# Optimization experiments

Measured on AMD Instinct MI355X. Metric: run time of the kernel, lower is better.

The kernel has to match this reference:

```python
import jax, jax.numpy as jnp
import numpy as np

N = 50000      # nodes
E = 600000     # edges
DIN = 128      # input_dim
H = 128        # hidden_dim
NH = 8         # heads
HD = H // NH   # head_dim = 16
OUT = 128      # output_dim
P = 20000      # pos/neg pair count
EPS = 1e-5


def setup_inputs() -> dict:
    key = jax.random.key(0)
    ks = jax.random.split(key, 20)
    s = 0.05
    inp = {
        "x": jax.random.normal(ks[0], (N, DIN), jnp.float32),
        "edge_index": jax.random.randint(ks[1], (2, E), 0, N),
        "drug_pos_ids": jax.random.randint(ks[2], (P,), 0, N),
        "target_pos_ids": jax.random.randint(ks[3], (P,), 0, N),
        "drug_neg_ids": jax.random.randint(ks[4], (P,), 0, N),
        "target_neg_ids": jax.random.randint(ks[5], (P,), 0, N),
        "adjacency_matrix": jnp.zeros((1,), jnp.float32),  # unused by forward
        # GCN weights stored [in, out]; biases [out]
        "gcn_w0": jax.random.normal(ks[6], (DIN, H), jnp.float32) * s,
        "gcn_b0": jnp.zeros((H,), jnp.float32),
        "gcn_w1": jax.random.normal(ks[7], (H, H), jnp.float32) * s,
        "gcn_b1": jnp.zeros((H,), jnp.float32),
        "gcn_w2": jax.random.normal(ks[8], (H, H), jnp.float32) * s,
        "gcn_b2": jnp.zeros((H,), jnp.float32),
        "wq": jax.random.normal(ks[9], (H, H), jnp.float32) * s,
        "wk": jax.random.normal(ks[10], (H, H), jnp.float32) * s,
        "wv": jax.random.normal(ks[11], (H, H), jnp.float32) * s,
        "ln_g": jnp.ones((H,), jnp.float32),   # shared LayerNorm (same instance reused)
        "ln_b": jnp.zeros((H,), jnp.float32),
        "out_w": jax.random.normal(ks[12], (H, OUT), jnp.float32) * s,
        "out_b": jnp.zeros((OUT,), jnp.float32),
    }
    return inp


def _layernorm(t, g, b):
    mu = t.mean(-1, keepdims=True)
    var = ((t - mu) ** 2).mean(-1, keepdims=True)
    return (t - mu) * jax.lax.rsqrt(var + EPS) * g + b


def reference(x, edge_index, drug_pos_ids, target_pos_ids, drug_neg_ids, target_neg_ids,
              adjacency_matrix, gcn_w0, gcn_b0, gcn_w1, gcn_b1, gcn_w2, gcn_b2,
              wq, wk, wv, ln_g, ln_b, out_w, out_b):
    num_nodes = x.shape[0]
    loop = jnp.arange(num_nodes)
    src = jnp.concatenate([edge_index[0], loop])  # add self-loops (PyG GCNConv default)
    dst = jnp.concatenate([edge_index[1], loop])
    deg = jax.ops.segment_sum(jnp.ones_like(dst, dtype=x.dtype), dst, num_segments=num_nodes)
    dinv = jnp.where(deg > 0, jax.lax.rsqrt(deg), 0.0)
    norm = dinv[src] * dinv[dst]  # [E+N]

    def gcn(h, W, b):
        hw = h @ W                                    # [N,H]
        msg = hw[src] * norm[:, None]                 # gather + scale  [E+N,H]
        return jax.ops.segment_sum(msg, dst, num_segments=num_nodes) + b

    cur = x
    embs = []
    for W, b in ((gcn_w0, gcn_b0), (gcn_w1, gcn_b1), (gcn_w2, gcn_b2)):
        new = jnp.maximum(gcn(cur, W, b), 0.0)
        new = _layernorm(new, ln_g, ln_b)
        # dropout is identity in eval mode
        cur = cur + new if cur.shape == new.shape else new
        embs.append(cur)
    emb = jnp.stack(embs, axis=0)  # [L,N,H]
    L = emb.shape[0]

    def split_heads(t):  # [L,N,H] -> [NH,N,L,HD]
        return t.reshape(L, num_nodes, NH, HD).transpose(2, 1, 0, 3)

    q = split_heads(emb @ wq)
    k = split_heads(emb @ wk)
    v = split_heads(emb @ wv)
    scores = jnp.einsum('hnld,hnmd->hnlm', q, k) / jnp.sqrt(jnp.float32(HD))
    attn = jax.nn.softmax(scores, axis=-1)  # dropout = identity in eval
    ctx = jnp.einsum('hnlm,hnmd->hnld', attn, v)          # [NH,N,L,HD]
    ctx = ctx.transpose(2, 1, 0, 3).reshape(L, num_nodes, H)

    z = _layernorm(ctx, ln_g, ln_b)
    z_last = z[-1] @ out_w + out_b  # [N,OUT]; z_D == z_T in original code
    return (z_last[drug_pos_ids], z_last[target_pos_ids],
            z_last[drug_neg_ids], z_last[target_neg_ids])
```

## Files before the change

kernel.cpp:

```cpp
#include <hip/hip_runtime.h>
#include <math.h>

using bf16x8 = __attribute__((ext_vector_type(8))) short;
using f32x4  = __attribute__((ext_vector_type(4))) float;

__device__ __forceinline__ unsigned short f2b(float f) {
  unsigned u = __float_as_uint(f);
  u += 0x7FFFu + ((u >> 16) & 1u);
  return (unsigned short)(u >> 16);
}
__device__ __forceinline__ float b2f(unsigned short h) {
  return __uint_as_float((unsigned)h << 16);
}
__device__ __forceinline__ float2 upk(unsigned u) {
  return make_float2(__uint_as_float(u << 16), __uint_as_float(u & 0xFFFF0000u));
}


__global__ void k_degree(const int* __restrict__ dst, int* __restrict__ degi, int E) {
  int e = blockIdx.x * blockDim.x + threadIdx.x;
  if (e < E) atomicAdd(&degi[dst[e]], 1);
}

__global__ void k_dinv(const int* __restrict__ degi, float* __restrict__ dinv, int n) {
  int i = blockIdx.x * blockDim.x + threadIdx.x;
  if (i < n) dinv[i] = rsqrtf((float)(degi[i] + 1));
}

__global__ __launch_bounds__(256)
void k_part(const int* __restrict__ deg, int* __restrict__ part, int n) {
  __shared__ int l[256];
  int tid = threadIdx.x, i = blockIdx.x * 256 + tid;
  l[tid] = (i < n) ? deg[i] : 0;
  __syncthreads();
  for (int s = 128; s; s >>= 1) { if (tid < s) l[tid] += l[tid + s]; __syncthreads(); }
  if (!tid) part[blockIdx.x] = l[0];
}

__global__ __launch_bounds__(1024)
void k_scanpart(int* __restrict__ part, int np, int* __restrict__ off_n) {
  __shared__ int l[1024];
  int tid = threadIdx.x;
  int v = (tid < np) ? part[tid] : 0;
  l[tid] = v;
  __syncthreads();
  for (int s = 1; s < 1024; s <<= 1) {
    int t = (tid >= s) ? l[tid - s] : 0;
    __syncthreads();
    l[tid] += t;
    __syncthreads();
  }
  if (tid < np) part[tid] = l[tid] - v;
  if (tid == np - 1) *off_n = l[tid];
}

__global__ __launch_bounds__(256)
void k_off(const int* __restrict__ deg, const int* __restrict__ part,
           int* __restrict__ off, int n) {
  __shared__ int l[256];
  int tid = threadIdx.x, i = blockIdx.x * 256 + tid;
  int v = (i < n) ? deg[i] : 0;
  l[tid] = v;
  __syncthreads();
  for (int s = 1; s < 256; s <<= 1) {
    int t = (tid >= s) ? l[tid - s] : 0;
    __syncthreads();
    l[tid] += t;
    __syncthreads();
  }
  if (i < n) off[i] = part[blockIdx.x] + l[tid] - v;
}

__global__ void k_scatter(const int* __restrict__ srcv, const int* __restrict__ dstv,
                          const float* __restrict__ dinv, const int* __restrict__ off,
                          int* __restrict__ cursor, int* __restrict__ csr_src,
                          float* __restrict__ csr_norm, int E) {
  int e = blockIdx.x * blockDim.x + threadIdx.x;
  if (e >= E) return;
  int d = dstv[e];
  int p = atomicAdd(&cursor[d], 1);
  int slot = off[d] + p;
  int s = srcv[e];
  csr_src[slot] = s;
  csr_norm[slot] = dinv[s] * dinv[d];
}


__global__ void k_cvtx(const float* __restrict__ x, unsigned short* __restrict__ xb,
                       long n4) {
  long t = (long)blockIdx.x * blockDim.x + threadIdx.x;
  if (t >= n4) return;
  float4 v = ((const float4*)x)[t];
  unsigned lo = (unsigned)f2b(v.x) | ((unsigned)f2b(v.y) << 16);
  unsigned hi = (unsigned)f2b(v.z) | ((unsigned)f2b(v.w) << 16);
  ((uint2*)xb)[t] = make_uint2(lo, hi);
}


__global__ __launch_bounds__(256)
void k_cvtw(const float* gw0, const float* gw1, const float* gw2,
            const float* wk, const float* wv, const float* wq, const float* ow,
            unsigned short* gwT0, unsigned short* gwT1, unsigned short* gwT2,
            unsigned short* wkvT, unsigned short* wqT, unsigned short* owT) {
  const float* src; unsigned short* dst;
  switch (blockIdx.y) {
    case 0: src = gw0; dst = gwT0; break;
    case 1: src = gw1; dst = gwT1; break;
    case 2: src = gw2; dst = gwT2; break;
    case 3: src = wk;  dst = wkvT; break;
    case 4: src = wv;  dst = wkvT + 128 * 128; break;
    case 5: src = wq;  dst = wqT; break;
    default: src = ow; dst = owT; break;
  }
  int t = blockIdx.x * 256 + threadIdx.x;
  int r = t >> 7, c = t & 127;
  dst[(long)c * 128 + r] = f2b(src[t]);
}


__global__ __launch_bounds__(128, 6)
void k_gcn_layer(const unsigned short* __restrict__ embp,
                 const int* __restrict__ off, const int* __restrict__ csr_src,
                 const float* __restrict__ csr_norm, const float* __restrict__ dinv,
                 const unsigned short* __restrict__ wT,
                 const float* __restrict__ bias,
                 const float* __restrict__ ln_g, const float* __restrict__ ln_b,
                 unsigned short* __restrict__ embo, int N) {
  __shared__ unsigned a_sw[16 * 64];
  __shared__ float lnsum[16][2], lnsq[16][2];

  int tid = threadIdx.x, lane = tid & 63, w = tid >> 6;
  int g = lane >> 4, c16 = lane & 15;
  long n0 = (long)blockIdx.x * 16;

  for (int t = 0; t < 8; ++t) {
    int row = w * 8 + t;
    long node = n0 + row;
    long nc = node < N ? node : N - 1;
    float dn = dinv[nc];
    int s0 = off[nc], s1 = off[nc + 1];
    float acc[8];
    {
      uint4 rs_ = *(const uint4*)&embp[nc * 128 + c16 * 8];
      float wgt = (g == 0) ? dn * dn : 0.f;
      float2 f;
      f = upk(rs_.x); acc[0] = f.x * wgt; acc[1] = f.y * wgt;
      f = upk(rs_.y); acc[2] = f.x * wgt; acc[3] = f.y * wgt;
      f = upk(rs_.z); acc[4] = f.x * wgt; acc[5] = f.y * wgt;
      f = upk(rs_.w); acc[6] = f.x * wgt; acc[7] = f.y * wgt;
    }
    for (int i = s0; i < s1; i += 16) {
      int id[4]; float nm[4];
#pragma unroll
      for (int u = 0; u < 4; ++u) {
        int j = i + u * 4 + g;
        int jj = j < s1 ? j : s1 - 1;
        id[u] = csr_src[jj];
        nm[u] = j < s1 ? csr_norm[jj] : 0.f;
      }
      uint4 rv[4];
#pragma unroll
      for (int u = 0; u < 4; ++u)
        rv[u] = *(const uint4*)&embp[(long)id[u] * 128 + c16 * 8];
#pragma unroll
      for (int u = 0; u < 4; ++u) {
        float2 f0 = upk(rv[u].x), f1 = upk(rv[u].y);
        float2 f2 = upk(rv[u].z), f3 = upk(rv[u].w);
        acc[0] += f0.x * nm[u]; acc[1] += f0.y * nm[u];
        acc[2] += f1.x * nm[u]; acc[3] += f1.y * nm[u];
        acc[4] += f2.x * nm[u]; acc[5] += f2.y * nm[u];
        acc[6] += f3.x * nm[u]; acc[7] += f3.y * nm[u];
      }
    }
#pragma unroll
    for (int k = 0; k < 8; ++k) {
      acc[k] += __shfl_xor(acc[k], 16);
      acc[k] += __shfl_xor(acc[k], 32);
    }
    if (g == 0) {
      unsigned* dst = (unsigned*)((char*)a_sw +
                      (row * 256 + ((c16 * 16) ^ ((row & 7) << 4))));
      dst[0] = (unsigned)f2b(acc[0]) | ((unsigned)f2b(acc[1]) << 16);
      dst[1] = (unsigned)f2b(acc[2]) | ((unsigned)f2b(acc[3]) << 16);
      dst[2] = (unsigned)f2b(acc[4]) | ((unsigned)f2b(acc[5]) << 16);
      dst[3] = (unsigned)f2b(acc[6]) | ((unsigned)f2b(acc[7]) << 16);
    }
  }
  __syncthreads();

  int lo = lane & 15, hi = lane >> 4;
  int cb0 = w * 64;
  f32x4 acc2[4] = {};
#pragma unroll
  for (int ks = 0; ks < 4; ++ks) {
    int k0 = ks * 32 + hi * 8;
    bf16x8 a = *(const bf16x8*)((char*)a_sw + lo * 256 + ((k0 * 2) ^ ((lo & 7) << 4)));
#pragma unroll
    for (int cf = 0; cf < 4; ++cf) {
      bf16x8 b = *(const bf16x8*)&wT[(long)(cb0 + cf * 16 + lo) * 128 + k0];
      acc2[cf] = __builtin_amdgcn_mfma_f32_16x16x32_bf16(a, b, acc2[cf], 0, 0, 0);
    }
  }

  float vreg[4][4];
#pragma unroll
  for (int j = 0; j < 4; ++j) {
    float s = 0.f, q = 0.f;
#pragma unroll
    for (int cf = 0; cf < 4; ++cf) {
      int col = cb0 + cf * 16 + lo;
      float v = fmaxf(acc2[cf][j] + bias[col], 0.f);
      vreg[cf][j] = v;
      s += v; q += v * v;
    }
#pragma unroll
    for (int m = 1; m < 16; m <<= 1) { s += __shfl_xor(s, m); q += __shfl_xor(q, m); }
    if (lo == 0) { lnsum[hi * 4 + j][w] = s; lnsq[hi * 4 + j][w] = q; }
  }
  __syncthreads();
#pragma unroll
  for (int j = 0; j < 4; ++j) {
    int row = hi * 4 + j;
    float sum = lnsum[row][0] + lnsum[row][1];
    float sq  = lnsq[row][0] + lnsq[row][1];
    float mu = sum * (1.f / 128.f);
    float var = sq * (1.f / 128.f) - mu * mu;
    float rs = rsqrtf(var + 1e-5f);
    long gr = n0 + row;
    if (gr < N) {
#pragma unroll
      for (int cf = 0; cf < 4; ++cf) {
        int col = cb0 + cf * 16 + lo;
        float z = (vreg[cf][j] - mu) * rs * ln_g[col] + ln_b[col]
                  + b2f(embp[gr * 128 + col]);
        embo[gr * 128 + col] = f2b(z);
      }
    }
  }
}


__global__ __launch_bounds__(256)
void k_attn_fused(const unsigned short* __restrict__ emb,
                  const unsigned short* __restrict__ wkvT,
                  const unsigned short* __restrict__ wqT,
                  const unsigned short* __restrict__ owT,
                  const float* __restrict__ ln_g, const float* __restrict__ ln_b,
                  const float* __restrict__ out_b,
                  float* __restrict__ zout, int N) {
  __shared__ unsigned short kvl[48 * 256];
  __shared__ unsigned short ql[16 * 128];
  __shared__ unsigned short zl[16 * 128];

  int tid = threadIdx.x, lane = tid & 63, w = tid >> 6;
  int lo = lane & 15, hi = lane >> 4;
  long n0 = (long)blockIdx.x * 16;
  long nr = n0 + lo; if (nr >= N) nr = N - 1;

  {
    int cb0 = w * 64;
    f32x4 acc[3][4] = {};
#pragma unroll
    for (int ks = 0; ks < 4; ++ks) {
      int k0 = ks * 32 + hi * 8;
      bf16x8 a[3];
#pragma unroll
      for (int l = 0; l < 3; ++l)
        a[l] = *(const bf16x8*)&emb[((long)l * N + nr) * 128 + k0];
#pragma unroll
      for (int cf = 0; cf < 4; ++cf) {
        bf16x8 b = *(const bf16x8*)&wkvT[(long)(cb0 + cf * 16 + lo) * 128 + k0];
#pragma unroll
        for (int l = 0; l < 3; ++l)
          acc[l][cf] = __builtin_amdgcn_mfma_f32_16x16x32_bf16(a[l], b, acc[l][cf], 0, 0, 0);
      }
    }
#pragma unroll
    for (int l = 0; l < 3; ++l)
#pragma unroll
      for (int cf = 0; cf < 4; ++cf)
#pragma unroll
        for (int j = 0; j < 4; ++j)
          kvl[(l * 16 + hi * 4 + j) * 256 + cb0 + cf * 16 + lo] = f2b(acc[l][cf][j]);
  }

  {
    int cq0 = w * 32;
    f32x4 aq[2] = {};
#pragma unroll
    for (int ks = 0; ks < 4; ++ks) {
      int k0 = ks * 32 + hi * 8;
      bf16x8 a = *(const bf16x8*)&emb[(2L * N + nr) * 128 + k0];
#pragma unroll
      for (int cf = 0; cf < 2; ++cf) {
        bf16x8 b = *(const bf16x8*)&wqT[(long)(cq0 + cf * 16 + lo) * 128 + k0];
        aq[cf] = __builtin_amdgcn_mfma_f32_16x16x32_bf16(a, b, aq[cf], 0, 0, 0);
      }
    }
#pragma unroll
    for (int cf = 0; cf < 2; ++cf)
#pragma unroll
      for (int j = 0; j < 4; ++j)
        ql[(hi * 4 + j) * 128 + cq0 + cf * 16 + lo] = f2b(aq[cf][j]);
  }
  __syncthreads();

  {
    const unsigned* kvu = (const unsigned*)kvl;
    const unsigned* qu  = (const unsigned*)ql;
    int c = lane * 2;
    float gx = ln_g[c], gy = ln_g[c + 1], bx = ln_b[c], by = ln_b[c + 1];
#pragma unroll
    for (int it = 0; it < 4; ++it) {
      int node = w * 4 + it;
      float2 q = upk(qu[node * 64 + lane]);
      float s[3], vx[3], vy[3];
#pragma unroll
      for (int m = 0; m < 3; ++m) {
        int row = m * 16 + node;
        float2 k = upk(kvu[row * 128 + lane]);
        float2 v = upk(kvu[row * 128 + 64 + lane]);
        float p = q.x * k.x + q.y * k.y;
        p += __shfl_xor(p, 1); p += __shfl_xor(p, 2); p += __shfl_xor(p, 4);
        s[m] = p * 0.25f;
        vx[m] = v.x; vy[m] = v.y;
      }
      float mx = fmaxf(s[0], fmaxf(s[1], s[2]));
      float e0 = __expf(s[0] - mx), e1 = __expf(s[1] - mx), e2 = __expf(s[2] - mx);
      float inv = 1.f / (e0 + e1 + e2);
      float cx = (e0 * vx[0] + e1 * vx[1] + e2 * vx[2]) * inv;
      float cy = (e0 * vy[0] + e1 * vy[1] + e2 * vy[2]) * inv;
      float sum = cx + cy, sq = cx * cx + cy * cy;
#pragma unroll
      for (int m = 1; m < 64; m <<= 1) { sum += __shfl_xor(sum, m); sq += __shfl_xor(sq, m); }
      float mu = sum * (1.f / 128.f);
      float var = sq * (1.f / 128.f) - mu * mu;
      float rs = rsqrtf(var + 1e-5f);
      unsigned pk = (unsigned)f2b((cx - mu) * rs * gx + bx) |
                    ((unsigned)f2b((cy - mu) * rs * gy + by) << 16);
      *(unsigned*)((char*)zl + node * 256 + ((lane * 4) ^ ((node & 7) << 4))) = pk;
    }
  }
  __syncthreads();

  {
    int co0 = w * 32;
    f32x4 ao[2] = {};
#pragma unroll
    for (int ks = 0; ks < 4; ++ks) {
      int k0 = ks * 32 + hi * 8;
      bf16x8 a = *(const bf16x8*)((const char*)zl + lo * 256 + (((k0 * 2) ^ ((lo & 7) << 4))));
#pragma unroll
      for (int cf = 0; cf < 2; ++cf) {
        bf16x8 b = *(const bf16x8*)&owT[(long)(co0 + cf * 16 + lo) * 128 + k0];
        ao[cf] = __builtin_amdgcn_mfma_f32_16x16x32_bf16(a, b, ao[cf], 0, 0, 0);
      }
    }
#pragma unroll
    for (int cf = 0; cf < 2; ++cf)
#pragma unroll
      for (int j = 0; j < 4; ++j) {
        long gn = n0 + hi * 4 + j;
        int col = co0 + cf * 16 + lo;
        if (gn < N) zout[gn * 128 + col] = ao[cf][j] + out_b[col];
      }
  }
}


__global__ void k_gather4(const float* __restrict__ zout,
                          const int* __restrict__ ids0, const int* __restrict__ ids1,
                          const int* __restrict__ ids2, const int* __restrict__ ids3,
                          float* __restrict__ outp, int rows) {
  int t = blockIdx.x * blockDim.x + threadIdx.x;
  if (t >= rows * 32) return;
  int s = blockIdx.y;
  const int* ids = (s == 0) ? ids0 : (s == 1) ? ids1 : (s == 2) ? ids2 : ids3;
  int row = t >> 5, c4 = t & 31;
  long id = ids[row];
  ((float4*)outp)[((long)s * rows + row) * 32 + c4] = ((const float4*)zout)[id * 32 + c4];
}


extern "C" void kernel_launch(void* const* d_in, const int* in_sizes, int n_in,
                              void* d_out, int out_size, void* d_ws, size_t ws_size,
                              hipStream_t stream) {
  const float* x = (const float*)d_in[0];
  const int* ei = (const int*)d_in[1];
  const int* ids[4] = {(const int*)d_in[2], (const int*)d_in[3],
                       (const int*)d_in[4], (const int*)d_in[5]};
  const float* gw[3] = {(const float*)d_in[7], (const float*)d_in[9], (const float*)d_in[11]};
  const float* gb[3] = {(const float*)d_in[8], (const float*)d_in[10], (const float*)d_in[12]};
  const float* wq = (const float*)d_in[13];
  const float* wk = (const float*)d_in[14];
  const float* wv = (const float*)d_in[15];
  const float* ln_g = (const float*)d_in[16];
  const float* ln_b = (const float*)d_in[17];
  const float* out_w = (const float*)d_in[18];
  const float* out_b = (const float*)d_in[19];

  const int N = in_sizes[0] / 128;
  const int E = in_sizes[1] / 2;
  const int P = in_sizes[2];

  char* w = (char*)d_ws;
  size_t o = 0;
  auto take = [&](size_t bytes) -> void* {
    void* p = w + o;
    o = (o + bytes + 255) & ~(size_t)255;
    return p;
  };
  int*   degi    = (int*)take((size_t)N * 4);
  int*   off     = (int*)take((size_t)(N + 1) * 4);
  int*   cursor  = (int*)take((size_t)N * 4);
  int*   part    = (int*)take(1024 * 4);
  float* dinv    = (float*)take((size_t)N * 4);
  int*   csr_src = (int*)take((size_t)E * 4);
  float* csr_nrm = (float*)take((size_t)E * 4);
  unsigned short* gwT0 = (unsigned short*)take(128 * 128 * 2);
  unsigned short* gwT1 = (unsigned short*)take(128 * 128 * 2);
  unsigned short* gwT2 = (unsigned short*)take(128 * 128 * 2);
  unsigned short* wkvT = (unsigned short*)take(256 * 128 * 2);
  unsigned short* wqT  = (unsigned short*)take(128 * 128 * 2);
  unsigned short* owT  = (unsigned short*)take(128 * 128 * 2);
  unsigned short* xbf  = (unsigned short*)take((size_t)N * 128 * 2);
  unsigned short* emball = (unsigned short*)take((size_t)3 * N * 128 * 2);
  float* zout = (float*)take((size_t)N * 128 * 4);
  (void)ws_size; (void)n_in; (void)out_size;

  hipMemsetAsync(degi, 0, (size_t)N * 4, stream);
  hipMemsetAsync(cursor, 0, (size_t)N * 4, stream);

  int eb = (E + 255) / 256;
  int nb = (N + 255) / 256;
  k_degree<<<eb, 256, 0, stream>>>(ei + E, degi, E);
  k_dinv<<<nb, 256, 0, stream>>>(degi, dinv, N);
  k_part<<<nb, 256, 0, stream>>>(degi, part, N);
  k_scanpart<<<1, 1024, 0, stream>>>(part, nb, off + N);
  k_off<<<nb, 256, 0, stream>>>(degi, part, off, N);
  k_scatter<<<eb, 256, 0, stream>>>(ei, ei + E, dinv, off, cursor, csr_src, csr_nrm, E);
  k_cvtw<<<dim3(64, 7), 256, 0, stream>>>(gw[0], gw[1], gw[2], wk, wv, wq, out_w,
                                          gwT0, gwT1, gwT2, wkvT, wqT, owT);
  long n4 = (long)N * 32;
  k_cvtx<<<(int)((n4 + 255) / 256), 256, 0, stream>>>(x, xbf, n4);

  unsigned short* gwT[3] = {gwT0, gwT1, gwT2};
  int lgrid = (N + 15) / 16;
  const unsigned short* prev = xbf;
  for (int l = 0; l < 3; ++l) {
    unsigned short* outp = emball + (size_t)l * N * 128;
    k_gcn_layer<<<lgrid, 128, 0, stream>>>(prev, off, csr_src, csr_nrm, dinv,
                                           gwT[l], gb[l], ln_g, ln_b, outp, N);
    prev = outp;
  }

  k_attn_fused<<<(N + 15) / 16, 256, 0, stream>>>(emball, wkvT, wqT, owT,
                                                  ln_g, ln_b, out_b, zout, N);

  float* outf = (float*)d_out;
  int gb2 = (P * 32 + 255) / 256;
  k_gather4<<<dim3(gb2, 4), 256, 0, stream>>>(zout, ids[0], ids[1], ids[2], ids[3],
                                              outf, P);
}
```

Before: 308.6 us.

## Rework GCN gather to 256-thread blocks, prefetch attention loads, swizzle LDS

The GCN layer kernel moves from 128 to 256 threads per block. Each wave now processes 4 rows, with every lane gathering 2 columns over 16 neighbours at once instead of 16-byte vectors split across 4 neighbour groups, and the MFMA/LayerNorm epilogue is split across 4 waves. The attention kernel double-buffers its K/V operand loads across k-steps, reuses the layer-2 embedding fragments for the Q projection instead of reloading them, and XOR-swizzles the kv/q LDS layout to reduce bank conflicts. The gather change trades larger vector loads for more independent loads in flight, and the extra prefetch registers may reduce occupancy.

```diff
diff --git a/kernel.cpp b/kernel.cpp
--- a/kernel.cpp
+++ b/kernel.cpp
@@ -118,7 +118,7 @@
 }
 
 
-__global__ __launch_bounds__(128, 6)
+__global__ __launch_bounds__(256)
 void k_gcn_layer(const unsigned short* __restrict__ embp,
                  const int* __restrict__ off, const int* __restrict__ csr_src,
                  const float* __restrict__ csr_norm, const float* __restrict__ dinv,
@@ -127,87 +127,64 @@
                  const float* __restrict__ ln_g, const float* __restrict__ ln_b,
                  unsigned short* __restrict__ embo, int N) {
   __shared__ unsigned a_sw[16 * 64];
-  __shared__ float lnsum[16][2], lnsq[16][2];
+  __shared__ float lnsum[16][4], lnsq[16][4];
 
   int tid = threadIdx.x, lane = tid & 63, w = tid >> 6;
-  int g = lane >> 4, c16 = lane & 15;
   long n0 = (long)blockIdx.x * 16;
-
-  for (int t = 0; t < 8; ++t) {
-    int row = w * 8 + t;
+  int c = lane * 2;
+
+  for (int t = 0; t < 4; ++t) {
+    int row = w * 4 + t;
     long node = n0 + row;
-    long nc = node < N ? node : N - 1;
-    float dn = dinv[nc];
-    int s0 = off[nc], s1 = off[nc + 1];
-    float acc[8];
-    {
-      uint4 rs_ = *(const uint4*)&embp[nc * 128 + c16 * 8];
-      float wgt = (g == 0) ? dn * dn : 0.f;
-      float2 f;
-      f = upk(rs_.x); acc[0] = f.x * wgt; acc[1] = f.y * wgt;
-      f = upk(rs_.y); acc[2] = f.x * wgt; acc[3] = f.y * wgt;
-      f = upk(rs_.z); acc[4] = f.x * wgt; acc[5] = f.y * wgt;
-      f = upk(rs_.w); acc[6] = f.x * wgt; acc[7] = f.y * wgt;
-    }
+    if (node >= N) node = N - 1;
+    float dn = dinv[node];
+    float2 acc = upk(*(const unsigned*)&embp[node * 128 + c]);
+    acc.x *= dn * dn; acc.y *= dn * dn;
+    int s0 = off[node], s1 = off[node + 1];
     for (int i = s0; i < s1; i += 16) {
-      int id[4]; float nm[4];
-#pragma unroll
-      for (int u = 0; u < 4; ++u) {
-        int j = i + u * 4 + g;
-        int jj = j < s1 ? j : s1 - 1;
-        id[u] = csr_src[jj];
-        nm[u] = j < s1 ? csr_norm[jj] : 0.f;
-      }
-      uint4 rv[4];
-#pragma unroll
-      for (int u = 0; u < 4; ++u)
-        rv[u] = *(const uint4*)&embp[(long)id[u] * 128 + c16 * 8];
-#pragma unroll
-      for (int u = 0; u < 4; ++u) {
-        float2 f0 = upk(rv[u].x), f1 = upk(rv[u].y);
-        float2 f2 = upk(rv[u].z), f3 = upk(rv[u].w);
-        acc[0] += f0.x * nm[u]; acc[1] += f0.y * nm[u];
-        acc[2] += f1.x * nm[u]; acc[3] += f1.y * nm[u];
-        acc[4] += f2.x * nm[u]; acc[5] += f2.y * nm[u];
-        acc[6] += f3.x * nm[u]; acc[7] += f3.y * nm[u];
-      }
-    }
-#pragma unroll
-    for (int k = 0; k < 8; ++k) {
-      acc[k] += __shfl_xor(acc[k], 16);
-      acc[k] += __shfl_xor(acc[k], 32);
-    }
-    if (g == 0) {
-      unsigned* dst = (unsigned*)((char*)a_sw +
-                      (row * 256 + ((c16 * 16) ^ ((row & 7) << 4))));
-      dst[0] = (unsigned)f2b(acc[0]) | ((unsigned)f2b(acc[1]) << 16);
-      dst[1] = (unsigned)f2b(acc[2]) | ((unsigned)f2b(acc[3]) << 16);
-      dst[2] = (unsigned)f2b(acc[4]) | ((unsigned)f2b(acc[5]) << 16);
-      dst[3] = (unsigned)f2b(acc[6]) | ((unsigned)f2b(acc[7]) << 16);
-    }
+      int idx[16]; float nrm[16];
+#pragma unroll
+      for (int u = 0; u < 16; ++u) {
+        int j = (i + u < s1) ? i + u : s1 - 1;
+        idx[u] = csr_src[j];
+        nrm[u] = (i + u < s1) ? csr_norm[j] : 0.f;
+      }
+      unsigned rv[16];
+#pragma unroll
+      for (int u = 0; u < 16; ++u)
+        rv[u] = *(const unsigned*)&embp[(long)idx[u] * 128 + c];
+#pragma unroll
+      for (int u = 0; u < 16; ++u) {
+        float2 f = upk(rv[u]);
+        acc.x += f.x * nrm[u];
+        acc.y += f.y * nrm[u];
+      }
+    }
+    unsigned pk = (unsigned)f2b(acc.x) | ((unsigned)f2b(acc.y) << 16);
+    *(unsigned*)((char*)a_sw + row * 256 + ((lane * 4) ^ ((row & 7) << 4))) = pk;
   }
   __syncthreads();
 
   int lo = lane & 15, hi = lane >> 4;
-  int cb0 = w * 64;
-  f32x4 acc2[4] = {};
+  int cb0 = w * 32;
+  f32x4 acc2[2] = {};
 #pragma unroll
   for (int ks = 0; ks < 4; ++ks) {
     int k0 = ks * 32 + hi * 8;
     bf16x8 a = *(const bf16x8*)((char*)a_sw + lo * 256 + ((k0 * 2) ^ ((lo & 7) << 4)));
 #pragma unroll
-    for (int cf = 0; cf < 4; ++cf) {
+    for (int cf = 0; cf < 2; ++cf) {
       bf16x8 b = *(const bf16x8*)&wT[(long)(cb0 + cf * 16 + lo) * 128 + k0];
       acc2[cf] = __builtin_amdgcn_mfma_f32_16x16x32_bf16(a, b, acc2[cf], 0, 0, 0);
     }
   }
 
-  float vreg[4][4];
+  float vreg[2][4];
 #pragma unroll
   for (int j = 0; j < 4; ++j) {
     float s = 0.f, q = 0.f;
 #pragma unroll
-    for (int cf = 0; cf < 4; ++cf) {
+    for (int cf = 0; cf < 2; ++cf) {
       int col = cb0 + cf * 16 + lo;
       float v = fmaxf(acc2[cf][j] + bias[col], 0.f);
       vreg[cf][j] = v;
@@ -221,15 +198,15 @@
 #pragma unroll
   for (int j = 0; j < 4; ++j) {
     int row = hi * 4 + j;
-    float sum = lnsum[row][0] + lnsum[row][1];
-    float sq  = lnsq[row][0] + lnsq[row][1];
+    float sum = lnsum[row][0] + lnsum[row][1] + lnsum[row][2] + lnsum[row][3];
+    float sq  = lnsq[row][0] + lnsq[row][1] + lnsq[row][2] + lnsq[row][3];
     float mu = sum * (1.f / 128.f);
     float var = sq * (1.f / 128.f) - mu * mu;
     float rs = rsqrtf(var + 1e-5f);
     long gr = n0 + row;
     if (gr < N) {
 #pragma unroll
-      for (int cf = 0; cf < 4; ++cf) {
+      for (int cf = 0; cf < 2; ++cf) {
         int col = cb0 + cf * 16 + lo;
         float z = (vreg[cf][j] - mu) * rs * ln_g[col] + ln_b[col]
                   + b2f(embp[gr * 128 + col]);
@@ -257,22 +234,45 @@
   long n0 = (long)blockIdx.x * 16;
   long nr = n0 + lo; if (nr >= N) nr = N - 1;
 
+  bf16x8 a2k[4];
+
   {
     int cb0 = w * 64;
     f32x4 acc[3][4] = {};
-#pragma unroll
-    for (int ks = 0; ks < 4; ++ks) {
-      int k0 = ks * 32 + hi * 8;
-      bf16x8 a[3];
+    bf16x8 a[3], b[4];
+    {
+      int k0 = hi * 8;
 #pragma unroll
       for (int l = 0; l < 3; ++l)
         a[l] = *(const bf16x8*)&emb[((long)l * N + nr) * 128 + k0];
 #pragma unroll
-      for (int cf = 0; cf < 4; ++cf) {
-        bf16x8 b = *(const bf16x8*)&wkvT[(long)(cb0 + cf * 16 + lo) * 128 + k0];
+      for (int cf = 0; cf < 4; ++cf)
+        b[cf] = *(const bf16x8*)&wkvT[(long)(cb0 + cf * 16 + lo) * 128 + k0];
+    }
+    a2k[0] = a[2];
+#pragma unroll
+    for (int ks = 0; ks < 4; ++ks) {
+      bf16x8 an[3], bn[4];
+      if (ks < 3) {
+        int k1 = (ks + 1) * 32 + hi * 8;
 #pragma unroll
         for (int l = 0; l < 3; ++l)
-          acc[l][cf] = __builtin_amdgcn_mfma_f32_16x16x32_bf16(a[l], b, acc[l][cf], 0, 0, 0);
+          an[l] = *(const bf16x8*)&emb[((long)l * N + nr) * 128 + k1];
+#pragma unroll
+        for (int cf = 0; cf < 4; ++cf)
+          bn[cf] = *(const bf16x8*)&wkvT[(long)(cb0 + cf * 16 + lo) * 128 + k1];
+      }
+#pragma unroll
+      for (int cf = 0; cf < 4; ++cf)
+#pragma unroll
+        for (int l = 0; l < 3; ++l)
+          acc[l][cf] = __builtin_amdgcn_mfma_f32_16x16x32_bf16(a[l], b[cf], acc[l][cf], 0, 0, 0);
+      if (ks < 3) {
+#pragma unroll
+        for (int l = 0; l < 3; ++l) a[l] = an[l];
+#pragma unroll
+        for (int cf = 0; cf < 4; ++cf) b[cf] = bn[cf];
+        a2k[ks + 1] = a[2];
       }
     }
 #pragma unroll
@@ -280,8 +280,12 @@
 #pragma unroll
       for (int cf = 0; cf < 4; ++cf)
 #pragma unroll
-        for (int j = 0; j < 4; ++j)
-          kvl[(l * 16 + hi * 4 + j) * 256 + cb0 + cf * 16 + lo] = f2b(acc[l][cf][j]);
+        for (int j = 0; j < 4; ++j) {
+          int row = l * 16 + hi * 4 + j;
+          int col = cb0 + cf * 16 + lo;
+          *(unsigned short*)((char*)kvl + row * 512 + ((col * 2) ^ (hi << 5))) =
+              f2b(acc[l][cf][j]);
+        }
   }
 
   {
@@ -290,36 +294,38 @@
 #pragma unroll
     for (int ks = 0; ks < 4; ++ks) {
       int k0 = ks * 32 + hi * 8;
-      bf16x8 a = *(const bf16x8*)&emb[(2L * N + nr) * 128 + k0];
 #pragma unroll
       for (int cf = 0; cf < 2; ++cf) {
         bf16x8 b = *(const bf16x8*)&wqT[(long)(cq0 + cf * 16 + lo) * 128 + k0];
-        aq[cf] = __builtin_amdgcn_mfma_f32_16x16x32_bf16(a, b, aq[cf], 0, 0, 0);
+        aq[cf] = __builtin_amdgcn_mfma_f32_16x16x32_bf16(a2k[ks], b, aq[cf], 0, 0, 0);
       }
     }
 #pragma unroll
     for (int cf = 0; cf < 2; ++cf)
 #pragma unroll
-      for (int j = 0; j < 4; ++j)
-        ql[(hi * 4 + j) * 128 + cq0 + cf * 16 + lo] = f2b(aq[cf][j]);
+      for (int j = 0; j < 4; ++j) {
+        int row = hi * 4 + j;
+        int col = cq0 + cf * 16 + lo;
+        *(unsigned short*)((char*)ql + row * 256 + ((col * 2) ^ (hi << 5))) =
+            f2b(aq[cf][j]);
+      }
   }
   __syncthreads();
 
   {
-    const unsigned* kvu = (const unsigned*)kvl;
-    const unsigned* qu  = (const unsigned*)ql;
     int c = lane * 2;
+    int rsw = w << 5;
     float gx = ln_g[c], gy = ln_g[c + 1], bx = ln_b[c], by = ln_b[c + 1];
 #pragma unroll
     for (int it = 0; it < 4; ++it) {
       int node = w * 4 + it;
-      float2 q = upk(qu[node * 64 + lane]);
+      float2 q = upk(*(const unsigned*)((const char*)ql + node * 256 + ((lane * 4) ^ rsw)));
       float s[3], vx[3], vy[3];
 #pragma unroll
       for (int m = 0; m < 3; ++m) {
         int row = m * 16 + node;
-        float2 k = upk(kvu[row * 128 + lane]);
-        float2 v = upk(kvu[row * 128 + 64 + lane]);
+        float2 k = upk(*(const unsigned*)((const char*)kvl + row * 512 + ((lane * 4) ^ rsw)));
+        float2 v = upk(*(const unsigned*)((const char*)kvl + row * 512 + ((256 + lane * 4) ^ rsw)));
         float p = q.x * k.x + q.y * k.y;
         p += __shfl_xor(p, 1); p += __shfl_xor(p, 2); p += __shfl_xor(p, 4);
         s[m] = p * 0.25f;
@@ -449,7 +455,7 @@
   const unsigned short* prev = xbf;
   for (int l = 0; l < 3; ++l) {
     unsigned short* outp = emball + (size_t)l * N * 128;
-    k_gcn_layer<<<lgrid, 128, 0, stream>>>(prev, off, csr_src, csr_nrm, dinv,
+    k_gcn_layer<<<lgrid, 256, 0, stream>>>(prev, off, csr_src, csr_nrm, dinv,
                                            gwT[l], gb[l], ln_g, ln_b, outp, N);
     prev = outp;
   }
```

Result: slower. 327.7 us (+6.2%).
